# Kernel tuning notes

Hardware: AMD Instinct MI355X
Metric: run time of the kernel (lower is better)

## Reference

```python
import jax, jax.numpy as jnp
import numpy as np

B, S, D, H, BLK = 2, 2048, 1024, 16, 128
DH = D // H
NB = S // BLK
EPS = 1e-5
NEG = -1e9


def _make_layout():
    i = np.arange(NB)[:, None]
    j = np.arange(NB)[None, :]
    # causal: local block diagonal + previous block + global first block column
    lay = ((j == i) | (j == i - 1) | (j == 0)) & (j <= i)
    return jnp.asarray(np.broadcast_to(lay, (H, NB, NB)).astype(np.int32))


def setup_inputs() -> dict:
    key = jax.random.key(0)
    ks = jax.random.split(key, 8)
    sd = 1.0 / np.sqrt(D)
    inp = {
        "x": jax.random.normal(ks[0], (B, S, D), jnp.float32),
        "ln1_g": jnp.ones((D,), jnp.float32),
        "ln1_b": jnp.zeros((D,), jnp.float32),
        "Wq": jax.random.normal(ks[1], (D, D), jnp.float32) * sd,
        "bq": jnp.zeros((D,), jnp.float32),
        "Wk": jax.random.normal(ks[2], (D, D), jnp.float32) * sd,
        "bk": jnp.zeros((D,), jnp.float32),
        "Wv": jax.random.normal(ks[3], (D, D), jnp.float32) * sd,
        "bv": jnp.zeros((D,), jnp.float32),
        "Wo": jax.random.normal(ks[4], (D, D), jnp.float32) * sd,
        "bo": jnp.zeros((D,), jnp.float32),
        "ln2_g": jnp.ones((D,), jnp.float32),
        "ln2_b": jnp.zeros((D,), jnp.float32),
        "W1": jax.random.normal(ks[5], (D, 4 * D), jnp.float32) * sd,
        "b1": jnp.zeros((4 * D,), jnp.float32),
        "W2": jax.random.normal(ks[6], (4 * D, D), jnp.float32) * (1.0 / np.sqrt(4 * D)),
        "b2": jnp.zeros((D,), jnp.float32),
        "layout": _make_layout(),
    }
    return inp


def _ln(x, g, b):
    m = jnp.mean(x, -1, keepdims=True)
    v = jnp.var(x, -1, keepdims=True)
    return (x - m) * jax.lax.rsqrt(v + EPS) * g + b


def reference(x, ln1_g, ln1_b, Wq, bq, Wk, bk, Wv, bv, Wo, bo,
              ln2_g, ln2_b, W1, b1, W2, b2, layout):
    # ---- pre-norm block-sparse multi-head attention + residual ----
    h = _ln(x, ln1_g, ln1_b)
    q = (h @ Wq + bq).reshape(B, S, H, DH).transpose(0, 2, 1, 3)
    k = (h @ Wk + bk).reshape(B, S, H, DH).transpose(0, 2, 1, 3)
    v = (h @ Wv + bv).reshape(B, S, H, DH).transpose(0, 2, 1, 3)

    # expand block layout [H,NB,NB] -> token mask [H,S,S], intersect with causal
    blk_mask = jnp.repeat(jnp.repeat(layout > 0, BLK, axis=1), BLK, axis=2)
    causal = jnp.tril(jnp.ones((S, S), bool))
    mask = blk_mask & causal  # [H,S,S]

    scale = DH ** -0.5
    scores = jnp.einsum("bhqd,bhkd->bhqk", q * scale, k)
    scores = jnp.where(mask[None], scores, NEG)
    att = jax.nn.softmax(scores, axis=-1)
    ctx = jnp.einsum("bhqk,bhkd->bhqd", att, v)
    ctx = ctx.transpose(0, 2, 1, 3).reshape(B, S, D)
    x = x + (ctx @ Wo + bo)

    # ---- pre-norm MLP (GeLU) + residual ----
    h2 = _ln(x, ln2_g, ln2_b)
    ff = jax.nn.gelu(h2 @ W1 + b1, approximate=False) @ W2 + b2
    return x + ff
```

## Files before the change

### kernel.cpp

```cpp
#include <hip/hip_runtime.h>

typedef unsigned short ushort;
typedef unsigned int uint;
typedef __attribute__((ext_vector_type(8))) short short8;
typedef __attribute__((ext_vector_type(4))) float floatx4;

#define DEV __device__ __forceinline__

DEV ushort f2bf(float f) {
    uint u = __float_as_uint(f);
    u += 0x7fffu + ((u >> 16) & 1u);
    return (ushort)(u >> 16);
}

DEV void load_lds16(const void* g, const void* l) {
    __builtin_amdgcn_global_load_lds(
        (const __attribute__((address_space(1))) void*)g,
        (__attribute__((address_space(3))) void*)l, 16, 0, 0);
}

template<int ROWS>
DEV void stage_tile(const ushort* g, int ldg, ushort* lds, int w, int lane) {
#pragma unroll
    for (int t = 0; t < ROWS / 32; ++t) {
        int row = t * 32 + w * 8 + (lane >> 3);
        int cg  = (lane & 7) ^ (row & 7);
        load_lds16(g + (size_t)row * ldg + cg * 8, lds + (t * 32 + w * 8) * 64);
    }
}

DEV short8 frag_ld(const ushort* lds, int row, int ks, int quad) {
    int slot = (ks * 4 + quad) ^ (row & 7);
    return *(const short8*)(lds + row * 64 + slot * 8);
}

__global__ __launch_bounds__(256) void prep_kernel(
    const float* __restrict__ Wq, const float* __restrict__ Wk,
    const float* __restrict__ Wv, const float* __restrict__ Wo,
    const float* __restrict__ W1, const float* __restrict__ W2,
    const float* __restrict__ bq, const float* __restrict__ bk,
    const float* __restrict__ bv,
    ushort* __restrict__ wqkvT, ushort* __restrict__ woT,
    ushort* __restrict__ w1T, ushort* __restrict__ w2T,
    float* __restrict__ bqkv,
    const float* __restrict__ x, const float* __restrict__ ln1g,
    const float* __restrict__ ln1b, ushort* __restrict__ hb) {
    __shared__ float t[64][65];
    int bid = blockIdx.x;
    int tid = threadIdx.x;
    if (bid >= 3072) {
        int row = bid - 3072;
        float4 v = ((const float4*)(x + (size_t)row * 1024))[tid];
        float s = v.x + v.y + v.z + v.w;
        float q = v.x * v.x + v.y * v.y + v.z * v.z + v.w * v.w;
#pragma unroll
        for (int m = 1; m < 64; m <<= 1) {
            s += __shfl_xor(s, m);
            q += __shfl_xor(q, m);
        }
        float* ss = &t[0][0];
        float* qs = &t[1][0];
        int w = tid >> 6;
        if ((tid & 63) == 0) { ss[w] = s; qs[w] = q; }
        __syncthreads();
        s = ss[0] + ss[1] + ss[2] + ss[3];
        q = qs[0] + qs[1] + qs[2] + qs[3];
        float mean = s * (1.0f / 1024.0f);
        float var  = q * (1.0f / 1024.0f) - mean * mean;
        float rs   = rsqrtf(var + 1e-5f);
        float4 gv = ((const float4*)ln1g)[tid];
        float4 bv4 = ((const float4*)ln1b)[tid];
        uint lo = f2bf((v.x - mean) * rs * gv.x + bv4.x) |
                  ((uint)f2bf((v.y - mean) * rs * gv.y + bv4.y) << 16);
        uint hi = f2bf((v.z - mean) * rs * gv.z + bv4.z) |
                  ((uint)f2bf((v.w - mean) * rs * gv.w + bv4.w) << 16);
        ((uint2*)(hb + (size_t)row * 1024))[tid] = make_uint2(lo, hi);
        return;
    }
    const float* in; ushort* out; int K, N, tx, ty;
    if (bid < 1024) {
        int m = bid >> 8, r = bid & 255;
        in  = m == 0 ? Wq : (m == 1 ? Wk : (m == 2 ? Wv : Wo));
        out = m < 3 ? wqkvT + (size_t)m * 1024 * 1024 : woT;
        K = 1024; N = 1024; tx = r & 15; ty = r >> 4;
    } else if (bid < 2048) {
        int r = bid - 1024; in = W1; out = w1T; K = 1024; N = 4096; tx = r & 63; ty = r >> 6;
    } else {
        int r = bid - 2048; in = W2; out = w2T; K = 4096; N = 1024; tx = r & 15; ty = r >> 4;
    }
    int txx = tid & 63, tyy = tid >> 6;
    int k0 = ty * 64, n0 = tx * 64;
#pragma unroll
    for (int r2 = tyy; r2 < 64; r2 += 4)
        t[r2][txx] = in[(size_t)(k0 + r2) * N + n0 + txx];
    __syncthreads();
#pragma unroll
    for (int r2 = tyy; r2 < 64; r2 += 4)
        out[(size_t)(n0 + r2) * K + k0 + txx] = f2bf(t[txx][r2]);
    if (bid < 12) {
        int i = bid * 256 + tid;
        bqkv[i] = i < 1024 ? bq[i] : (i < 2048 ? bk[i - 1024] : bv[i - 2048]);
    }
}

__global__ __launch_bounds__(256) void ln_kernel(const float* __restrict__ x,
                                                 const float* __restrict__ g,
                                                 const float* __restrict__ bb,
                                                 ushort* __restrict__ out) {
    int row = blockIdx.x, tid = threadIdx.x;
    float4 v = ((const float4*)(x + (size_t)row * 1024))[tid];
    float s = v.x + v.y + v.z + v.w;
    float q = v.x * v.x + v.y * v.y + v.z * v.z + v.w * v.w;
#pragma unroll
    for (int m = 1; m < 64; m <<= 1) {
        s += __shfl_xor(s, m);
        q += __shfl_xor(q, m);
    }
    __shared__ float ss[4], qs[4];
    int w = tid >> 6;
    if ((tid & 63) == 0) { ss[w] = s; qs[w] = q; }
    __syncthreads();
    s = ss[0] + ss[1] + ss[2] + ss[3];
    q = qs[0] + qs[1] + qs[2] + qs[3];
    float mean = s * (1.0f / 1024.0f);
    float var  = q * (1.0f / 1024.0f) - mean * mean;
    float rs   = rsqrtf(var + 1e-5f);
    float4 gv = ((const float4*)g)[tid];
    float4 bv = ((const float4*)bb)[tid];
    uint lo = f2bf((v.x - mean) * rs * gv.x + bv.x) |
              ((uint)f2bf((v.y - mean) * rs * gv.y + bv.y) << 16);
    uint hi = f2bf((v.z - mean) * rs * gv.z + bv.z) |
              ((uint)f2bf((v.w - mean) * rs * gv.w + bv.w) << 16);
    ((uint2*)(out + (size_t)row * 1024))[tid] = make_uint2(lo, hi);
}

__global__ __launch_bounds__(256) void combine2(const float* __restrict__ p,
                                                const float* __restrict__ res,
                                                const float* __restrict__ bias,
                                                float* __restrict__ out,
                                                int MN, int N) {
    int idx = (blockIdx.x * 256 + threadIdx.x) * 4;
    float4 a = *(const float4*)(p + idx);
    float4 b = *(const float4*)(p + MN + idx);
    float4 r = *(const float4*)(res + idx);
    float4 bi = *(const float4*)(bias + (idx & (N - 1)));
    float4 o;
    o.x = a.x + b.x + r.x + bi.x;
    o.y = a.y + b.y + r.y + bi.y;
    o.z = a.z + b.z + r.z + bi.z;
    o.w = a.w + b.w + r.w + bi.w;
    *(float4*)(out + idx) = o;
}

template<int MODE>
__global__ __launch_bounds__(256, 2) void gemm_db(const ushort* __restrict__ A,
                                                  const ushort* __restrict__ Bt,
                                                  const float* __restrict__ bias,
                                                  const float* __restrict__ res,
                                                  void* __restrict__ outp,
                                                  int M, int N, int K, int ksplit,
                                                  int stx_n, int per_xcd) {
    constexpr int BUFE = 256 * 64;
    __shared__ ushort smem[2 * BUFE];
    int tid = threadIdx.x, w = tid >> 6, lane = tid & 63;
    int quad = lane >> 4, l15 = lane & 15;
    int wm = w >> 1, wn = w & 1;

    int flat = blockIdx.x;
    int xcd = flat & 7, slot = flat >> 3;
    int st = xcd * per_xcd + (slot >> 4);
    int li = slot & 15;
    int bx = (st % stx_n) * 4 + (li & 3);
    int by = (st / stx_n) * 4 + (li >> 2);
    int m0 = by * 128, n0 = bx * 128;
    int sk = blockIdx.y, KS = K / ksplit;
    int kbeg = sk * KS, kend = kbeg + KS;

    const ushort* Ab = A + (size_t)m0 * K;
    const ushort* Bb = Bt + (size_t)n0 * K;

    stage_tile<128>(Ab + kbeg, K, smem, w, lane);
    stage_tile<128>(Bb + kbeg, K, smem + 128 * 64, w, lane);

    int sl0 = (quad ^ (l15 & 7)) * 16;
    int oa0 = (wm * 64 + l15) * 128 + sl0;          int oa1 = oa0 ^ 64;
    int ob0 = 16384 + (wn * 64 + l15) * 128 + sl0;  int ob1 = ob0 ^ 64;

    floatx4 acc[4][4] = {};
    int cur = 0;
    for (int k0 = kbeg; k0 < kend; k0 += 64) {
        __syncthreads();
        if (k0 + 64 < kend) {
            ushort* nb = smem + (cur ^ 1) * BUFE;
            stage_tile<128>(Ab + k0 + 64, K, nb, w, lane);
            stage_tile<128>(Bb + k0 + 64, K, nb + 128 * 64, w, lane);
        }
#pragma unroll
        for (int ks = 0; ks < 2; ++ks) {
            int oa = ks ? oa1 : oa0, ob = ks ? ob1 : ob0;
            short8 af[4], bfr[4];
#pragma unroll
            for (int i = 0; i < 4; ++i)
                af[i] = *(const short8*)((const char*)smem + oa + i * 2048);
#pragma unroll
            for (int j = 0; j < 4; ++j)
                bfr[j] = *(const short8*)((const char*)smem + ob + j * 2048);
#pragma unroll
            for (int i = 0; i < 4; ++i)
#pragma unroll
                for (int j = 0; j < 4; ++j)
                    acc[i][j] = __builtin_amdgcn_mfma_f32_16x16x32_bf16(bfr[j], af[i], acc[i][j], 0, 0, 0);
        }
        oa0 ^= 32768; oa1 ^= 32768; ob0 ^= 32768; ob1 ^= 32768;
        cur ^= 1;
    }

    ushort* Sb = smem;
    float*  Sf = (float*)smem;
    int rl  = wm * 16 + l15;
    int rl2 = tid >> 3, c8 = tid & 7;
    if (MODE <= 1) {
#pragma unroll
        for (int i = 0; i < 4; ++i) {
            __syncthreads();
#pragma unroll
            for (int j = 0; j < 4; ++j) {
                int col = wn * 64 + j * 16 + quad * 4;
                float4 bv4 = *(const float4*)(bias + n0 + col);
                float v0 = acc[i][j][0] + bv4.x, v1 = acc[i][j][1] + bv4.y;
                float v2 = acc[i][j][2] + bv4.z, v3 = acc[i][j][3] + bv4.w;
                if (MODE == 1) {
                    v0 = 0.5f * v0 * (1.0f + erff(v0 * 0.70710678118f));
                    v1 = 0.5f * v1 * (1.0f + erff(v1 * 0.70710678118f));
                    v2 = 0.5f * v2 * (1.0f + erff(v2 * 0.70710678118f));
                    v3 = 0.5f * v3 * (1.0f + erff(v3 * 0.70710678118f));
                }
                uint lo = f2bf(v0) | ((uint)f2bf(v1) << 16);
                uint hi = f2bf(v2) | ((uint)f2bf(v3) << 16);
                *(uint2*)(Sb + rl * 136 + col) = make_uint2(lo, hi);
            }
            __syncthreads();
            int grow = m0 + (rl2 >> 4) * 64 + i * 16 + (rl2 & 15);
            short8 d0 = *(short8*)(Sb + rl2 * 136 + c8 * 8);
            short8 d1 = *(short8*)(Sb + rl2 * 136 + 64 + c8 * 8);
            if (MODE == 1) {
                ushort* op = (ushort*)outp + (size_t)grow * N + n0 + c8 * 8;
                *(short8*)op = d0;
                *(short8*)(op + 64) = d1;
            } else {
                int b = grow >> 11, s = grow & 2047;
                int which = n0 >> 10, nbase = n0 & 1023;
                int h0 = nbase >> 6;
                size_t a0 = (size_t)which * 4194304 +
                            (((size_t)(b * 16 + h0)) * 2048 + s) * 64 + c8 * 8;
                size_t a1 = (size_t)which * 4194304 +
                            (((size_t)(b * 16 + h0 + 1)) * 2048 + s) * 64 + c8 * 8;
                *(short8*)((ushort*)outp + a0) = d0;
                *(short8*)((ushort*)outp + a1) = d1;
            }
        }
    } else {
#pragma unroll
        for (int i = 0; i < 4; ++i) {
#pragma unroll
            for (int hh = 0; hh < 2; ++hh) {
                __syncthreads();
                if (wn == hh) {
#pragma unroll
                    for (int j = 0; j < 4; ++j) {
                        float4 wv;
                        wv.x = acc[i][j][0]; wv.y = acc[i][j][1];
                        wv.z = acc[i][j][2]; wv.w = acc[i][j][3];
                        *(float4*)(Sf + rl * 68 + j * 16 + quad * 4) = wv;
                    }
                }
                __syncthreads();
                int grow = m0 + (rl2 >> 4) * 64 + i * 16 + (rl2 & 15);
                int gc = n0 + hh * 64 + c8 * 8;
                float4 u0 = *(float4*)(Sf + rl2 * 68 + c8 * 8);
                float4 u1 = *(float4*)(Sf + rl2 * 68 + c8 * 8 + 4);
                if (MODE == 3) {
                    float* op = (float*)outp + (size_t)sk * M * N + (size_t)grow * N + gc;
                    *(float4*)op = u0;
                    *(float4*)(op + 4) = u1;
                } else {
                    float4 b0 = *(const float4*)(bias + gc);
                    float4 b1 = *(const float4*)(bias + gc + 4);
                    const float* rp = res + (size_t)grow * N + gc;
                    float4 r0 = *(const float4*)rp;
                    float4 r1 = *(const float4*)(rp + 4);
                    float4 o0, o1;
                    o0.x = u0.x + b0.x + r0.x; o0.y = u0.y + b0.y + r0.y;
                    o0.z = u0.z + b0.z + r0.z; o0.w = u0.w + b0.w + r0.w;
                    o1.x = u1.x + b1.x + r1.x; o1.y = u1.y + b1.y + r1.y;
                    o1.z = u1.z + b1.z + r1.z; o1.w = u1.w + b1.w + r1.w;
                    float* op = (float*)outp + (size_t)grow * N + gc;
                    *(float4*)op = o0;
                    *(float4*)(op + 4) = o1;
                }
            }
        }
    }
}

__global__ __launch_bounds__(256) void attn_kernel(const ushort* __restrict__ qg,
                                                   const ushort* __restrict__ kg,
                                                   const ushort* __restrict__ vg,
                                                   ushort* __restrict__ ctx) {
    __shared__ ushort Qs[64 * 64];
    __shared__ ushort Ks[128 * 64];
    __shared__ ushort Vs[64 * 136];
    __shared__ ushort Ps[64 * 136];
    int iq2 = blockIdx.x, h = blockIdx.y, b = blockIdx.z;
    int tid = threadIdx.x, w = tid >> 6, lane = tid & 63;
    int quad = lane >> 4, l15 = lane & 15;
    int iq = iq2 >> 1;

    const ushort* qp    = qg + ((size_t)(b * 16 + h) * 2048 + iq2 * 64) * 64;
    const ushort* kbase = kg + (size_t)(b * 16 + h) * 2048 * 64;
    const ushort* vbase = vg + (size_t)(b * 16 + h) * 2048 * 64;

    stage_tile<64>(qp, 64, Qs, w, lane);

    floatx4 o[4] = {};
    float mi[4], li[4];
#pragma unroll
    for (int r = 0; r < 4; ++r) { mi[r] = -1e30f; li[r] = 0.0f; }

    int jbs[3];
    int nj = 0;
    jbs[nj++] = 0;
    if (iq > 1) jbs[nj++] = iq - 1;
    if (iq > 0) jbs[nj++] = iq;

    for (int ji = 0; ji < nj; ++ji) {
        int jb = jbs[ji];
        __syncthreads();
        stage_tile<128>(kbase + (size_t)jb * 128 * 64, 64, Ks, w, lane);
        {
            int dh = tid & 63, sg = tid >> 6;
            const ushort* vp = vbase + (size_t)jb * 128 * 64;
#pragma unroll
            for (int cc = 0; cc < 8; ++cc) {
                int s0 = sg * 32 + cc * 4;
                ushort e0 = vp[(s0 + 0) * 64 + dh];
                ushort e1 = vp[(s0 + 1) * 64 + dh];
                ushort e2 = vp[(s0 + 2) * 64 + dh];
                ushort e3 = vp[(s0 + 3) * 64 + dh];
                uint lo = e0 | ((uint)e1 << 16), hi = e2 | ((uint)e3 << 16);
                *(uint2*)(Vs + dh * 136 + s0) = make_uint2(lo, hi);
            }
        }
        __syncthreads();

        floatx4 sacc[8] = {};
#pragma unroll
        for (int ks = 0; ks < 2; ++ks) {
            short8 af = frag_ld(Qs, w * 16 + l15, ks, quad);
            short8 bf8[8];
#pragma unroll
            for (int nt = 0; nt < 8; ++nt) bf8[nt] = frag_ld(Ks, nt * 16 + l15, ks, quad);
#pragma unroll
            for (int nt = 0; nt < 8; ++nt)
                sacc[nt] = __builtin_amdgcn_mfma_f32_16x16x32_bf16(af, bf8[nt], sacc[nt], 0, 0, 0);
        }

        float rowmax[4] = {-1e30f, -1e30f, -1e30f, -1e30f};
        bool diag = (jb == iq);
        int rowL0 = (iq2 & 1) * 64 + w * 16 + quad * 4;
#pragma unroll
        for (int nt = 0; nt < 8; ++nt) {
#pragma unroll
            for (int r = 0; r < 4; ++r) {
                float xv = sacc[nt][r] * 0.125f;
                if (diag && (nt * 16 + l15 > rowL0 + r)) xv = -1e30f;
                sacc[nt][r] = xv;
                rowmax[r] = fmaxf(rowmax[r], xv);
            }
        }
#pragma unroll
        for (int r = 0; r < 4; ++r)
#pragma unroll
            for (int m = 1; m < 16; m <<= 1)
                rowmax[r] = fmaxf(rowmax[r], __shfl_xor(rowmax[r], m));

        float alpha[4], rsum[4];
#pragma unroll
        for (int r = 0; r < 4; ++r) {
            float mnew = fmaxf(mi[r], rowmax[r]);
            alpha[r] = __expf(mi[r] - mnew);
            mi[r] = mnew;
            rsum[r] = 0.0f;
        }
#pragma unroll
        for (int nt = 0; nt < 8; ++nt) {
#pragma unroll
            for (int r = 0; r < 4; ++r) {
                float p = __expf(sacc[nt][r] - mi[r]);
                rsum[r] += p;
                Ps[(w * 16 + quad * 4 + r) * 136 + nt * 16 + l15] = f2bf(p);
            }
        }
#pragma unroll
        for (int r = 0; r < 4; ++r) {
#pragma unroll
            for (int m = 1; m < 16; m <<= 1) rsum[r] += __shfl_xor(rsum[r], m);
            li[r] = li[r] * alpha[r] + rsum[r];
        }
#pragma unroll
        for (int nt = 0; nt < 4; ++nt)
#pragma unroll
            for (int r = 0; r < 4; ++r) o[nt][r] *= alpha[r];

#pragma unroll
        for (int ks2 = 0; ks2 < 4; ++ks2) {
            short8 ap = *(const short8*)(Ps + (w * 16 + l15) * 136 + ks2 * 32 + quad * 8);
            short8 bv4[4];
#pragma unroll
            for (int nt = 0; nt < 4; ++nt)
                bv4[nt] = *(const short8*)(Vs + (nt * 16 + l15) * 136 + ks2 * 32 + quad * 8);
#pragma unroll
            for (int nt = 0; nt < 4; ++nt)
                o[nt] = __builtin_amdgcn_mfma_f32_16x16x32_bf16(ap, bv4[nt], o[nt], 0, 0, 0);
        }
    }
#pragma unroll
    for (int nt = 0; nt < 4; ++nt) {
#pragma unroll
        for (int r = 0; r < 4; ++r) {
            int srow = iq2 * 64 + w * 16 + quad * 4 + r;
            float val = o[nt][r] / li[r];
            ctx[((size_t)b * 2048 + srow) * 1024 + h * 64 + nt * 16 + l15] = f2bf(val);
        }
    }
}

extern "C" void kernel_launch(void* const* d_in, const int* in_sizes, int n_in,
                              void* d_out, int out_size, void* d_ws, size_t ws_size,
                              hipStream_t stream) {
    (void)in_sizes; (void)n_in; (void)out_size; (void)ws_size;
    const float* x    = (const float*)d_in[0];
    const float* ln1g = (const float*)d_in[1];
    const float* ln1b = (const float*)d_in[2];
    const float* Wq   = (const float*)d_in[3];
    const float* bq   = (const float*)d_in[4];
    const float* Wk   = (const float*)d_in[5];
    const float* bk   = (const float*)d_in[6];
    const float* Wv   = (const float*)d_in[7];
    const float* bv   = (const float*)d_in[8];
    const float* Wo   = (const float*)d_in[9];
    const float* bo   = (const float*)d_in[10];
    const float* ln2g = (const float*)d_in[11];
    const float* ln2b = (const float*)d_in[12];
    const float* W1   = (const float*)d_in[13];
    const float* b1   = (const float*)d_in[14];
    const float* W2   = (const float*)d_in[15];
    const float* b2   = (const float*)d_in[16];

    char* ws = (char*)d_ws;
    size_t off = 0;
    auto alloc = [&](size_t bytes) {
        char* p = ws + off;
        off += (bytes + 255) & ~(size_t)255;
        return p;
    };
    ushort* wqkvT = (ushort*)alloc((size_t)3072 * 1024 * 2);
    ushort* woT   = (ushort*)alloc((size_t)1024 * 1024 * 2);
    ushort* w1T   = (ushort*)alloc((size_t)1024 * 4096 * 2);
    ushort* w2T   = (ushort*)alloc((size_t)4096 * 1024 * 2);
    float*  bqkv  = (float*)alloc((size_t)3072 * 4);
    ushort* hb    = (ushort*)alloc((size_t)4096 * 1024 * 2);
    ushort* qkvb  = (ushort*)alloc((size_t)3 * 4096 * 1024 * 2);
    ushort* ctx   = (ushort*)alloc((size_t)4096 * 1024 * 2);
    float*  x1    = (float*)alloc((size_t)4096 * 1024 * 4);
    ushort* h2    = (ushort*)alloc((size_t)4096 * 1024 * 2);
    ushort* ub    = (ushort*)alloc((size_t)4096 * 4096 * 2);
    float* w2p = (float*)hb;

    prep_kernel<<<7168, 256, 0, stream>>>(Wq, Wk, Wv, Wo, W1, W2, bq, bk, bv,
                                          wqkvT, woT, w1T, w2T, bqkv,
                                          x, ln1g, ln1b, hb);

    gemm_db<0><<<dim3(768, 1), 256, 0, stream>>>(hb, wqkvT, bqkv, nullptr, qkvb,
                                                 4096, 3072, 1024, 1, 6, 6);

    attn_kernel<<<dim3(32, 16, 2), 256, 0, stream>>>(qkvb, qkvb + 4194304,
                                                     qkvb + 2 * 4194304, ctx);

    gemm_db<2><<<dim3(256, 1), 256, 0, stream>>>(ctx, woT, bo, x, x1,
                                                 4096, 1024, 1024, 1, 2, 2);

    ln_kernel<<<4096, 256, 0, stream>>>(x1, ln2g, ln2b, h2);

    gemm_db<1><<<dim3(1024, 1), 256, 0, stream>>>(h2, w1T, b1, nullptr, ub,
                                                  4096, 4096, 1024, 1, 8, 8);

    gemm_db<3><<<dim3(256, 2), 256, 0, stream>>>(ub, w2T, b2, nullptr, w2p,
                                                 4096, 1024, 4096, 2, 2, 2);
    combine2<<<4096, 256, 0, stream>>>(w2p, x1, b2, (float*)d_out,
                                       4096 * 1024, 1024);
}
```

Baseline: 324.2 us.

## Process 128 query rows per attention block to reuse staged K/V tiles

Each attention workgroup now handles a full 128-row query block as two 64-row halves instead of a single 64-row half. The K tile and the transposed V tile are staged into LDS once and used by both halves, so each K/V block is loaded half as often and the strided, scalar V transpose runs half as many times. In exchange the grid shrinks from 1024 to 512 workgroups, each doing twice the serial work, and registers rise from keeping two sets of output accumulators. That lowers parallelism across CUs on a kernel that is only a small part of the full layer.

```diff
diff --git a/kernel.cpp b/kernel.cpp
--- a/kernel.cpp
+++ b/kernel.cpp
@@ -307,25 +307,26 @@
                                                    const ushort* __restrict__ kg,
                                                    const ushort* __restrict__ vg,
                                                    ushort* __restrict__ ctx) {
-    __shared__ ushort Qs[64 * 64];
+    __shared__ ushort Qs[128 * 64];
     __shared__ ushort Ks[128 * 64];
     __shared__ ushort Vs[64 * 136];
     __shared__ ushort Ps[64 * 136];
-    int iq2 = blockIdx.x, h = blockIdx.y, b = blockIdx.z;
+    int iq = blockIdx.x, h = blockIdx.y, b = blockIdx.z;
     int tid = threadIdx.x, w = tid >> 6, lane = tid & 63;
     int quad = lane >> 4, l15 = lane & 15;
-    int iq = iq2 >> 1;
-
-    const ushort* qp    = qg + ((size_t)(b * 16 + h) * 2048 + iq2 * 64) * 64;
+
+    const ushort* qp    = qg + ((size_t)(b * 16 + h) * 2048 + iq * 128) * 64;
     const ushort* kbase = kg + (size_t)(b * 16 + h) * 2048 * 64;
     const ushort* vbase = vg + (size_t)(b * 16 + h) * 2048 * 64;
 
-    stage_tile<64>(qp, 64, Qs, w, lane);
-
-    floatx4 o[4] = {};
-    float mi[4], li[4];
-#pragma unroll
-    for (int r = 0; r < 4; ++r) { mi[r] = -1e30f; li[r] = 0.0f; }
+    stage_tile<128>(qp, 64, Qs, w, lane);
+
+    floatx4 o[2][4] = {};
+    float mi[2][4], li[2][4];
+#pragma unroll
+    for (int hf = 0; hf < 2; ++hf)
+#pragma unroll
+        for (int r = 0; r < 4; ++r) { mi[hf][r] = -1e30f; li[hf][r] = 0.0f; }
 
     int jbs[3];
     int nj = 0;
@@ -352,87 +353,92 @@
             }
         }
         __syncthreads();
-
-        floatx4 sacc[8] = {};
-#pragma unroll
-        for (int ks = 0; ks < 2; ++ks) {
-            short8 af = frag_ld(Qs, w * 16 + l15, ks, quad);
-            short8 bf8[8];
-#pragma unroll
-            for (int nt = 0; nt < 8; ++nt) bf8[nt] = frag_ld(Ks, nt * 16 + l15, ks, quad);
-#pragma unroll
-            for (int nt = 0; nt < 8; ++nt)
-                sacc[nt] = __builtin_amdgcn_mfma_f32_16x16x32_bf16(af, bf8[nt], sacc[nt], 0, 0, 0);
-        }
-
-        float rowmax[4] = {-1e30f, -1e30f, -1e30f, -1e30f};
         bool diag = (jb == iq);
-        int rowL0 = (iq2 & 1) * 64 + w * 16 + quad * 4;
-#pragma unroll
-        for (int nt = 0; nt < 8; ++nt) {
+
+#pragma unroll
+        for (int hf = 0; hf < 2; ++hf) {
+            floatx4 sacc[8] = {};
+#pragma unroll
+            for (int ks = 0; ks < 2; ++ks) {
+                short8 af = frag_ld(Qs, hf * 64 + w * 16 + l15, ks, quad);
+                short8 bf8[8];
+#pragma unroll
+                for (int nt = 0; nt < 8; ++nt) bf8[nt] = frag_ld(Ks, nt * 16 + l15, ks, quad);
+#pragma unroll
+                for (int nt = 0; nt < 8; ++nt)
+                    sacc[nt] = __builtin_amdgcn_mfma_f32_16x16x32_bf16(af, bf8[nt], sacc[nt], 0, 0, 0);
+            }
+
+            float rowmax[4] = {-1e30f, -1e30f, -1e30f, -1e30f};
+            int rowL0 = hf * 64 + w * 16 + quad * 4;
+#pragma unroll
+            for (int nt = 0; nt < 8; ++nt) {
+#pragma unroll
+                for (int r = 0; r < 4; ++r) {
+                    float xv = sacc[nt][r] * 0.125f;
+                    if (diag && (nt * 16 + l15 > rowL0 + r)) xv = -1e30f;
+                    sacc[nt][r] = xv;
+                    rowmax[r] = fmaxf(rowmax[r], xv);
+                }
+            }
+#pragma unroll
+            for (int r = 0; r < 4; ++r)
+#pragma unroll
+                for (int m = 1; m < 16; m <<= 1)
+                    rowmax[r] = fmaxf(rowmax[r], __shfl_xor(rowmax[r], m));
+
+            float alpha[4], rsum[4];
 #pragma unroll
             for (int r = 0; r < 4; ++r) {
-                float xv = sacc[nt][r] * 0.125f;
-                if (diag && (nt * 16 + l15 > rowL0 + r)) xv = -1e30f;
-                sacc[nt][r] = xv;
-                rowmax[r] = fmaxf(rowmax[r], xv);
-            }
-        }
-#pragma unroll
-        for (int r = 0; r < 4; ++r)
-#pragma unroll
-            for (int m = 1; m < 16; m <<= 1)
-                rowmax[r] = fmaxf(rowmax[r], __shfl_xor(rowmax[r], m));
-
-        float alpha[4], rsum[4];
-#pragma unroll
-        for (int r = 0; r < 4; ++r) {
-            float mnew = fmaxf(mi[r], rowmax[r]);
-            alpha[r] = __expf(mi[r] - mnew);
-            mi[r] = mnew;
-            rsum[r] = 0.0f;
-        }
-#pragma unroll
-        for (int nt = 0; nt < 8; ++nt) {
+                float mnew = fmaxf(mi[hf][r], rowmax[r]);
+                alpha[r] = __expf(mi[hf][r] - mnew);
+                mi[hf][r] = mnew;
+                rsum[r] = 0.0f;
+            }
+#pragma unroll
+            for (int nt = 0; nt < 8; ++nt) {
+#pragma unroll
+                for (int r = 0; r < 4; ++r) {
+                    float p = __expf(sacc[nt][r] - mi[hf][r]);
+                    rsum[r] += p;
+                    Ps[(w * 16 + quad * 4 + r) * 136 + nt * 16 + l15] = f2bf(p);
+                }
+            }
 #pragma unroll
             for (int r = 0; r < 4; ++r) {
-                float p = __expf(sacc[nt][r] - mi[r]);
-                rsum[r] += p;
-                Ps[(w * 16 + quad * 4 + r) * 136 + nt * 16 + l15] = f2bf(p);
-            }
-        }
-#pragma unroll
-        for (int r = 0; r < 4; ++r) {
-#pragma unroll
-            for (int m = 1; m < 16; m <<= 1) rsum[r] += __shfl_xor(rsum[r], m);
-            li[r] = li[r] * alpha[r] + rsum[r];
-        }
-#pragma unroll
-        for (int nt = 0; nt < 4; ++nt)
-#pragma unroll
-            for (int r = 0; r < 4; ++r) o[nt][r] *= alpha[r];
-
-#pragma unroll
-        for (int ks2 = 0; ks2 < 4; ++ks2) {
-            short8 ap = *(const short8*)(Ps + (w * 16 + l15) * 136 + ks2 * 32 + quad * 8);
-            short8 bv4[4];
+#pragma unroll
+                for (int m = 1; m < 16; m <<= 1) rsum[r] += __shfl_xor(rsum[r], m);
+                li[hf][r] = li[hf][r] * alpha[r] + rsum[r];
+            }
 #pragma unroll
             for (int nt = 0; nt < 4; ++nt)
-                bv4[nt] = *(const short8*)(Vs + (nt * 16 + l15) * 136 + ks2 * 32 + quad * 8);
-#pragma unroll
-            for (int nt = 0; nt < 4; ++nt)
-                o[nt] = __builtin_amdgcn_mfma_f32_16x16x32_bf16(ap, bv4[nt], o[nt], 0, 0, 0);
-        }
-    }
-#pragma unroll
-    for (int nt = 0; nt < 4; ++nt) {
-#pragma unroll
-        for (int r = 0; r < 4; ++r) {
-            int srow = iq2 * 64 + w * 16 + quad * 4 + r;
-            float val = o[nt][r] / li[r];
-            ctx[((size_t)b * 2048 + srow) * 1024 + h * 64 + nt * 16 + l15] = f2bf(val);
-        }
-    }
+#pragma unroll
+                for (int r = 0; r < 4; ++r) o[hf][nt][r] *= alpha[r];
+
+#pragma unroll
+            for (int ks2 = 0; ks2 < 4; ++ks2) {
+                short8 ap = *(const short8*)(Ps + (w * 16 + l15) * 136 + ks2 * 32 + quad * 8);
+                short8 bv4[4];
+#pragma unroll
+                for (int nt = 0; nt < 4; ++nt)
+                    bv4[nt] = *(const short8*)(Vs + (nt * 16 + l15) * 136 + ks2 * 32 + quad * 8);
+#pragma unroll
+                for (int nt = 0; nt < 4; ++nt)
+                    o[hf][nt] = __builtin_amdgcn_mfma_f32_16x16x32_bf16(ap, bv4[nt], o[hf][nt], 0, 0, 0);
+            }
+        }
+    }
+#pragma unroll
+    for (int hf = 0; hf < 2; ++hf)
+#pragma unroll
+        for (int nt = 0; nt < 4; ++nt) {
+#pragma unroll
+            for (int r = 0; r < 4; ++r) {
+                int srow = iq * 128 + hf * 64 + w * 16 + quad * 4 + r;
+                float val = o[hf][nt][r] / li[hf][r];
+                ctx[((size_t)b * 2048 + srow) * 1024 + h * 64 + nt * 16 + l15] = f2bf(val);
+            }
+        }
 }
 
 extern "C" void kernel_launch(void* const* d_in, const int* in_sizes, int n_in,
@@ -484,7 +490,7 @@
     gemm_db<0><<<dim3(768, 1), 256, 0, stream>>>(hb, wqkvT, bqkv, nullptr, qkvb,
                                                  4096, 3072, 1024, 1, 6, 6);
 
-    attn_kernel<<<dim3(32, 16, 2), 256, 0, stream>>>(qkvb, qkvb + 4194304,
+    attn_kernel<<<dim3(16, 16, 2), 256, 0, stream>>>(qkvb, qkvb + 4194304,
                                                      qkvb + 2 * 4194304, ctx);
 
     gemm_db<2><<<dim3(256, 1), 256, 0, stream>>>(ctx, woT, bo, x, x1,
```

Result: slower. 335.7 us (+3.5%).
